# Optimization experiments

Measured on AMD Instinct MI355X. Metric: run time of the kernel, lower is better.

Reference implementation:

```python
import jax, jax.numpy as jnp
import numpy as np

B, D, RES, NSLOTS, NITERS = 32, 256, 64, 8, 3
NTOK = RES * RES
SCALE = D ** -0.5
EPS = 1e-8
LN_EPS = 1e-5


def _ln(x, g, b, axes=(-1,)):
    m = x.mean(axes, keepdims=True)
    v = x.var(axes, keepdims=True)
    return (x - m) / jnp.sqrt(v + LN_EPS) * g + b


def _build_grid(res):
    xy = jnp.linspace(0.0, 1.0, res)
    xx, yy = jnp.meshgrid(xy, xy, indexing='ij')
    g = jnp.stack([xx, yy], axis=-1)[None]  # [1,res,res,2]
    return jnp.concatenate([g, 1.0 - g], axis=-1)  # [1,res,res,4]


GRID = _build_grid(RES)


def setup_inputs() -> dict:
    key = jax.random.key(0)
    ks = iter(jax.random.split(key, 48))
    w = lambda shp: 0.02 * jax.random.normal(next(ks), shp, jnp.float32)
    z = lambda shp: jnp.zeros(shp, jnp.float32)
    o = lambda shp: jnp.ones(shp, jnp.float32)
    return dict(
        x=jax.random.normal(next(ks), (B, D, RES, RES), jnp.float32),
        eps_noise=jax.random.normal(next(ks), (B, NSLOTS, D), jnp.float32),
        pos_w=w((4, D)), pos_b=z((D,)),
        enc_g=o((NTOK, D)), enc_b=z((NTOK, D)),
        fm_w1=w((D, D)), fm_b1=z((D,)), fm_w2=w((D, D)), fm_b2=z((D,)),
        in_g=o((D,)), in_b=z((D,)),
        q_w=w((D, D)), q_b=z((D,)),
        k_w=w((D, D)), k_b=z((D,)),
        v_w=w((D, D)), v_b=z((D,)),
        gru_wih=w((D, 3 * D)), gru_whh=w((D, 3 * D)), gru_bih=z((3 * D,)), gru_bhh=z((3 * D,)),
        pre_g=o((D,)), pre_b=z((D,)),
        st_w1=w((D, D)), st_b1=z((D,)), st_w2=w((D, D)), st_b2=z((D,)),
        slot_g=o((D,)), slot_b=z((D,)),
        slots_loc=w((1, D)),
        slots_logscale=jax.random.uniform(next(ks), (1, D), jnp.float32),
    )


def reference(x, eps_noise, pos_w, pos_b, enc_g, enc_b, fm_w1, fm_b1, fm_w2, fm_b2,
              in_g, in_b, q_w, q_b, k_w, k_b, v_w, v_b,
              gru_wih, gru_whh, gru_bih, gru_bhh, pre_g, pre_b,
              st_w1, st_b1, st_w2, st_b2, slot_g, slot_b, slots_loc, slots_logscale):
    # SoftPositionEmbed: x + Linear(grid) permuted to NCHW
    pos = GRID @ pos_w + pos_b                       # [1,res,res,D]
    h = x + jnp.transpose(pos, (0, 3, 1, 2))         # [B,D,res,res]
    tokens = h.reshape(B, D, NTOK).transpose(0, 2, 1)  # [B,NTOK,D]
    # encoder_norm: LayerNorm over [NTOK, D] jointly
    tokens = _ln(tokens, enc_g, enc_b, axes=(-2, -1))
    tokens = jax.nn.relu(tokens @ fm_w1 + fm_b1)
    tokens = jax.nn.relu(tokens @ fm_w2 + fm_b2)
    tokens = _ln(tokens, in_g, in_b)                 # norm_input
    k = tokens @ k_w + k_b                           # [B,NTOK,D]
    v = tokens @ v_w + v_b
    # stochastic initial slots (non-variational branch)
    slots = slots_loc[None] + jnp.exp(slots_logscale)[None] * eps_noise  # [B,S,D]
    for _ in range(NITERS):
        prev = slots
        s = _ln(slots, slot_g, slot_b)               # norm_slots
        q = s @ q_w + q_b
        dots = jnp.einsum('bid,bjd->bij', q, k) * SCALE  # [B,S,NTOK]
        attn = jax.nn.softmax(dots, axis=1) + EPS    # softmax over SLOT axis
        attn = attn / attn.sum(-1, keepdims=True)    # renormalize over tokens
        upd = jnp.einsum('bij,bjd->bid', attn, v)    # [B,S,D]
        # GRUCell(update, prev) — torch gate order r,z,n
        gi = upd @ gru_wih + gru_bih
        gh = prev @ gru_whh + gru_bhh
        ir, iz, inn = jnp.split(gi, 3, axis=-1)
        hr, hz, hn = jnp.split(gh, 3, axis=-1)
        r = jax.nn.sigmoid(ir + hr)
        zt = jax.nn.sigmoid(iz + hz)
        n = jnp.tanh(inn + r * hn)
        slots = (1.0 - zt) * n + zt * prev
        # residual MLP: slots += slot_transformation(norm_pre_ff(slots))
        ff = _ln(slots, pre_g, pre_b)
        ff = jax.nn.relu(ff @ st_w1 + st_b1)
        ff = jax.nn.relu(ff @ st_w2 + st_b2)
        slots = slots + ff
    return slots
```

## Files before the change

### kernel.cpp

```cpp
#include <hip/hip_runtime.h>
#include <hip/hip_bf16.h>

typedef __attribute__((ext_vector_type(8))) short short8;
typedef __attribute__((ext_vector_type(4))) float f32x4;

#define DEVI static __device__ __forceinline__

DEVI ushort f2bf(float f) {
  union { __hip_bfloat16 h; ushort u; } c; c.h = __float2bfloat16(f); return c.u;
}
DEVI float bf2f(ushort u) {
  union { __hip_bfloat16 h; ushort u; } c; c.u = u; return __bfloat162float(c.h);
}

DEVI void blk_reduce2(float& a, float& b) {
  #pragma unroll
  for (int m = 1; m < 64; m <<= 1) {
    a += __shfl_xor(a, m);
    b += __shfl_xor(b, m);
  }
  __shared__ float sc[8];
  int tid = threadIdx.x, w = tid >> 6;
  if ((tid & 63) == 0) { sc[w * 2] = a; sc[w * 2 + 1] = b; }
  __syncthreads();
  if (tid == 0) {
    sc[0] = sc[0] + sc[2] + sc[4] + sc[6];
    sc[1] = sc[1] + sc[3] + sc[5] + sc[7];
  }
  __syncthreads();
  a = sc[0]; b = sc[1];
  __syncthreads();
}

__global__ void kw_kernel(const float* w0, const float* w1, const float* w2, const float* w3,
                          ushort* wT, float* bstats) {
  int widx = blockIdx.y;
  const float* src = (widx == 0) ? w0 : (widx == 1) ? w1 : (widx == 2) ? w2 : w3;
  ushort* dst = wT + (size_t)widx * 65536;
  int tile = blockIdx.x;
  int k0 = (tile >> 2) * 64, n0 = (tile & 3) * 64;
  __shared__ float t[64][65];
  int tid = threadIdx.x;
  int r = tid >> 2, c0 = (tid & 3) * 16;
  #pragma unroll
  for (int j = 0; j < 16; j += 4) {
    float4 v = *reinterpret_cast<const float4*>(src + (size_t)(k0 + r) * 256 + n0 + c0 + j);
    t[r][c0 + j + 0] = v.x; t[r][c0 + j + 1] = v.y;
    t[r][c0 + j + 2] = v.z; t[r][c0 + j + 3] = v.w;
  }
  __syncthreads();
  ushort buf[16];
  #pragma unroll
  for (int j = 0; j < 16; j++) buf[j] = f2bf(t[c0 + j][r]);
  size_t o = (size_t)(n0 + r) * 256 + k0 + c0;
  *reinterpret_cast<uint4*>(dst + o) = *reinterpret_cast<uint4*>(&buf[0]);
  *reinterpret_cast<uint4*>(dst + o + 8) = *reinterpret_cast<uint4*>(&buf[8]);
  if (blockIdx.x == 0 && blockIdx.y == 0 && tid < 64) bstats[tid] = 0.f;
}

__global__ void k1_stats(const float* x, const float* pos_w, const float* pos_b, float* bstats) {
  int b = blockIdx.y, blk = blockIdx.x, tid = threadIdx.x;
  const float* xb = x + (size_t)b * 1048576;
  float s = 0.f, sq = 0.f;
  for (int i = 0; i < 16; i++) {
    int e4 = blk * 4096 + i * 256 + tid;
    int e = e4 * 4;
    int d = e >> 12, t = e & 4095;
    int ii = t >> 6, j0 = t & 63;
    float xx = ii * (1.f / 63.f);
    float c0 = pos_w[512 + d] + pos_w[768 + d] + pos_b[d];
    float cx = pos_w[d] - pos_w[512 + d];
    float cy = pos_w[256 + d] - pos_w[768 + d];
    float4 v = reinterpret_cast<const float4*>(xb)[e4];
    float base = c0 + xx * cx;
    #pragma unroll
    for (int j = 0; j < 4; j++) {
      float yy = (j0 + j) * (1.f / 63.f);
      float h = (&v.x)[j] + base + yy * cy;
      s += h; sq += h * h;
    }
  }
  blk_reduce2(s, sq);
  if (tid == 0) {
    atomicAdd(&bstats[b * 2], s);
    atomicAdd(&bstats[b * 2 + 1], sq);
  }
}

__global__ void k2_tokens(const float* x, const float* pos_w, const float* pos_b,
                          const float* enc_g, const float* enc_b, const float* bstats,
                          ushort* t0) {
  int tcx = blockIdx.x;
  int dcx = blockIdx.y;
  int b = blockIdx.z;
  int tid = threadIdx.x;
  float mean = bstats[b * 2] * (1.f / 1048576.f);
  float var = bstats[b * 2 + 1] * (1.f / 1048576.f) - mean * mean;
  float rstd = rsqrtf(var + 1e-5f);
  __shared__ float tt[64][65];
  const float* xb = x + (size_t)b * 1048576;
  float xx = tcx * (1.f / 63.f);
  #pragma unroll
  for (int it = 0; it < 4; it++) {
    int idx = tid + it * 256;
    int dl = idx >> 4, f4 = idx & 15;
    int d = dcx * 64 + dl;
    float c0 = pos_w[512 + d] + pos_w[768 + d] + pos_b[d];
    float cx = pos_w[d] - pos_w[512 + d];
    float cy = pos_w[256 + d] - pos_w[768 + d];
    float4 v = *reinterpret_cast<const float4*>(xb + (size_t)d * 4096 + tcx * 64 + f4 * 4);
    float base = c0 + xx * cx;
    #pragma unroll
    for (int j = 0; j < 4; j++) {
      float yy = (f4 * 4 + j) * (1.f / 63.f);
      tt[f4 * 4 + j][dl] = (&v.x)[j] + base + yy * cy;
    }
  }
  __syncthreads();
  int t_l = tid >> 2, dc = (tid & 3) * 16;
  int t = tcx * 64 + t_l;
  ushort ob[16];
  #pragma unroll
  for (int j = 0; j < 16; j++) {
    int d = dcx * 64 + dc + j;
    float h = (tt[t_l][dc + j] - mean) * rstd;
    h = h * enc_g[(size_t)t * 256 + d] + enc_b[(size_t)t * 256 + d];
    ob[j] = f2bf(h);
  }
  size_t o = (size_t)(b * 4096 + t) * 256 + dcx * 64 + dc;
  *reinterpret_cast<uint4*>(t0 + o) = *reinterpret_cast<uint4*>(&ob[0]);
  *reinterpret_cast<uint4*>(t0 + o + 8) = *reinterpret_cast<uint4*>(&ob[8]);
}

template <bool RELU>
__global__ __launch_bounds__(512) void gemm_kernel(const ushort* __restrict__ A,
                                                   const ushort* __restrict__ WT,
                                                   const float* __restrict__ bias,
                                                   ushort* __restrict__ C) {
  __shared__ ushort As[128 * 72];
  __shared__ ushort Bs[256 * 72];
  int tid = threadIdx.x;
  int r0 = blockIdx.x * 128;
  int w = tid >> 6, lane = tid & 63;
  int wr = w >> 2, wc = w & 3;
  f32x4 acc[4][4];
  #pragma unroll
  for (int m = 0; m < 4; m++)
    #pragma unroll
    for (int n = 0; n < 4; n++) acc[m][n] = (f32x4)(0.f);

  for (int ks = 0; ks < 4; ks++) {
    int k0 = ks * 64;
    __syncthreads();
    #pragma unroll
    for (int i = 0; i < 2; i++) {
      int idx = tid + i * 512;
      int r = idx >> 3, cc = idx & 7;
      uint4 v = *reinterpret_cast<const uint4*>(A + (size_t)(r0 + r) * 256 + k0 + cc * 8);
      *reinterpret_cast<uint4*>(&As[r * 72 + cc * 8]) = v;
    }
    #pragma unroll
    for (int i = 0; i < 4; i++) {
      int idx = tid + i * 512;
      int r = idx >> 3, cc = idx & 7;
      uint4 v = *reinterpret_cast<const uint4*>(WT + (size_t)r * 256 + k0 + cc * 8);
      *reinterpret_cast<uint4*>(&Bs[r * 72 + cc * 8]) = v;
    }
    __syncthreads();
    #pragma unroll
    for (int ksub = 0; ksub < 2; ksub++) {
      int kk = ksub * 32 + (lane >> 4) * 8;
      short8 af[4], bf[4];
      #pragma unroll
      for (int m = 0; m < 4; m++)
        af[m] = *reinterpret_cast<const short8*>(&As[(wr * 64 + m * 16 + (lane & 15)) * 72 + kk]);
      #pragma unroll
      for (int n = 0; n < 4; n++)
        bf[n] = *reinterpret_cast<const short8*>(&Bs[(wc * 64 + n * 16 + (lane & 15)) * 72 + kk]);
      #pragma unroll
      for (int m = 0; m < 4; m++)
        #pragma unroll
        for (int n = 0; n < 4; n++)
          acc[m][n] = __builtin_amdgcn_mfma_f32_16x16x32_bf16(af[m], bf[n], acc[m][n], 0, 0, 0);
    }
  }
  #pragma unroll
  for (int m = 0; m < 4; m++) {
    int row = r0 + wr * 64 + m * 16 + ((lane >> 4) << 2);
    #pragma unroll
    for (int n = 0; n < 4; n++) {
      int col = wc * 64 + n * 16 + (lane & 15);
      float bv = bias[col];
      #pragma unroll
      for (int q = 0; q < 4; q++) {
        float v = acc[m][n][q] + bv;
        if (RELU) v = fmaxf(v, 0.f);
        C[(size_t)(row + q) * 256 + col] = f2bf(v);
      }
    }
  }
}

__global__ void lnrow_kernel(ushort* t, const float* g, const float* bta) {
  int row = blockIdx.x * 4 + (threadIdx.x >> 6);
  int lane = threadIdx.x & 63;
  ushort* p = t + (size_t)row * 256 + lane * 4;
  uint2 v = *reinterpret_cast<const uint2*>(p);
  ushort us[4]; *reinterpret_cast<uint2*>(us) = v;
  float f[4];
  float s = 0.f, sq = 0.f;
  #pragma unroll
  for (int j = 0; j < 4; j++) { f[j] = bf2f(us[j]); s += f[j]; sq += f[j] * f[j]; }
  #pragma unroll
  for (int m = 1; m < 64; m <<= 1) { s += __shfl_xor(s, m); sq += __shfl_xor(sq, m); }
  float mean = s * (1.f / 256.f);
  float var = sq * (1.f / 256.f) - mean * mean;
  float rstd = rsqrtf(var + 1e-5f);
  float4 gv = *reinterpret_cast<const float4*>(g + lane * 4);
  float4 bv = *reinterpret_cast<const float4*>(bta + lane * 4);
  #pragma unroll
  for (int j = 0; j < 4; j++) us[j] = f2bf((f[j] - mean) * rstd * (&gv.x)[j] + (&bv.x)[j]);
  *reinterpret_cast<uint2*>(p) = *reinterpret_cast<uint2*>(us);
}

__global__ void kslots_kernel(const float* eps, const float* loc, const float* lsc, float* slots) {
  int i = blockIdx.x * 256 + threadIdx.x;
  int d = i & 255;
  slots[i] = loc[d] + expf(lsc[d]) * eps[i];
}

__global__ void ka_kernel(const float* slots, const float* sg, const float* sb,
                          const float* qw, const float* qb, ushort* qT, float* attn_sum) {
  int s = blockIdx.x;
  int b = blockIdx.y;
  int tid = threadIdx.x;
  ushort* qrow = qT + ((size_t)b * 16 + s) * 256;
  if (s >= 8) { qrow[tid] = 0; return; }
  __shared__ float sn[256];
  float xv = slots[((size_t)b * 8 + s) * 256 + tid];
  float a = xv, sq = xv * xv;
  blk_reduce2(a, sq);
  float mean = a * (1.f / 256.f);
  float var = sq * (1.f / 256.f) - mean * mean;
  float rstd = rsqrtf(var + 1e-5f);
  sn[tid] = (xv - mean) * rstd * sg[tid] + sb[tid];
  __syncthreads();
  float acc = qb[tid];
  for (int d = 0; d < 256; d++) acc = fmaf(sn[d], qw[(size_t)d * 256 + tid], acc);
  qrow[tid] = f2bf(acc * 0.0625f);
  if (tid == 0) attn_sum[b * 8 + s] = 0.f;
}

__global__ __launch_bounds__(256) void kb_kernel(const ushort* __restrict__ kmat,
                                                 const ushort* __restrict__ qT,
                                                 float* __restrict__ attn,
                                                 float* __restrict__ attn_sum,
                                                 float* __restrict__ upd) {
  int tcx = blockIdx.x;
  int b = blockIdx.y;
  int tid = threadIdx.x, w = tid >> 6, lane = tid & 63;
  if (tid < 128) upd[(size_t)b * 2048 + tcx * 128 + tid] = 0.f;
  __shared__ ushort Ks[256 * 72];
  const ushort* kbase = kmat + ((size_t)b * 4096 + tcx * 256) * 256;
  const ushort* qbase = qT + (size_t)b * 16 * 256;
  f32x4 acc[4];
  #pragma unroll
  for (int m = 0; m < 4; m++) acc[m] = (f32x4)(0.f);
  for (int ks = 0; ks < 4; ks++) {
    int k0 = ks * 64;
    __syncthreads();
    #pragma unroll
    for (int i = 0; i < 8; i++) {
      int idx = tid + i * 256;
      int r = idx >> 3, cc = idx & 7;
      *reinterpret_cast<uint4*>(&Ks[r * 72 + cc * 8]) =
          *reinterpret_cast<const uint4*>(kbase + (size_t)r * 256 + k0 + cc * 8);
    }
    __syncthreads();
    #pragma unroll
    for (int ksub = 0; ksub < 2; ksub++) {
      int kk = ksub * 32 + (lane >> 4) * 8;
      short8 bq = *reinterpret_cast<const short8*>(qbase + (lane & 15) * 256 + k0 + kk);
      #pragma unroll
      for (int m = 0; m < 4; m++) {
        short8 af = *reinterpret_cast<const short8*>(&Ks[(w * 64 + m * 16 + (lane & 15)) * 72 + kk]);
        acc[m] = __builtin_amdgcn_mfma_f32_16x16x32_bf16(af, bq, acc[m], 0, 0, 0);
      }
    }
  }
  bool valid = (lane & 15) < 8;
  float lsum = 0.f;
  int srow = (lane >> 4) * 4;
  #pragma unroll
  for (int m = 0; m < 4; m++) {
    #pragma unroll
    for (int q = 0; q < 4; q++) {
      float d = acc[m][q];
      float mv = valid ? d : -1e30f;
      #pragma unroll
      for (int msk = 1; msk < 16; msk <<= 1) mv = fmaxf(mv, __shfl_xor(mv, msk));
      float e = valid ? expf(d - mv) : 0.f;
      float ssum = e;
      #pragma unroll
      for (int msk = 1; msk < 16; msk <<= 1) ssum += __shfl_xor(ssum, msk);
      if (valid) {
        float av = e / ssum + 1e-8f;
        int t = tcx * 256 + w * 64 + m * 16 + srow + q;
        attn[((size_t)b * 4096 + t) * 8 + (lane & 15)] = av;
        lsum += av;
      }
    }
  }
  lsum += __shfl_xor(lsum, 16);
  lsum += __shfl_xor(lsum, 32);
  __shared__ float wsum[4][16];
  if (lane < 16) wsum[w][lane] = lsum;
  __syncthreads();
  if (tid < 8) {
    float tot = wsum[0][tid] + wsum[1][tid] + wsum[2][tid] + wsum[3][tid];
    atomicAdd(&attn_sum[b * 8 + tid], tot);
  }
}

__global__ __launch_bounds__(256) void kc_kernel(const ushort* __restrict__ vmat,
                                                 const float* __restrict__ attn,
                                                 float* __restrict__ upd) {
  int tcx = blockIdx.x;
  int b = blockIdx.y;
  int tid = threadIdx.x, g = tid >> 6, lane = tid & 63;
  __shared__ float at[64][8];
  __shared__ float red[4][8][256];
  float acc[8][4];
  #pragma unroll
  for (int s = 0; s < 8; s++)
    #pragma unroll
    for (int j = 0; j < 4; j++) acc[s][j] = 0.f;
  const ushort* vb = vmat + ((size_t)b * 4096 + tcx * 512) * 256;
  const float* ab = attn + ((size_t)b * 4096 + tcx * 512) * 8;
  for (int tile = 0; tile < 8; tile++) {
    __syncthreads();
    if (tid < 128)
      *reinterpret_cast<float4*>(&at[0][0] + tid * 4) =
          *reinterpret_cast<const float4*>(ab + tile * 512 + tid * 4);
    __syncthreads();
    for (int ti = 0; ti < 16; ti++) {
      int tl = g * 16 + ti;
      uint2 vv = *reinterpret_cast<const uint2*>(vb + (size_t)(tile * 64 + tl) * 256 + lane * 4);
      ushort us[4]; *reinterpret_cast<uint2*>(us) = vv;
      float vf[4];
      #pragma unroll
      for (int j = 0; j < 4; j++) vf[j] = bf2f(us[j]);
      #pragma unroll
      for (int s = 0; s < 8; s++) {
        float a = at[tl][s];
        #pragma unroll
        for (int j = 0; j < 4; j++) acc[s][j] = fmaf(a, vf[j], acc[s][j]);
      }
    }
  }
  #pragma unroll
  for (int s = 0; s < 8; s++) {
    float4 v4; v4.x = acc[s][0]; v4.y = acc[s][1]; v4.z = acc[s][2]; v4.w = acc[s][3];
    *reinterpret_cast<float4*>(&red[g][s][lane * 4]) = v4;
  }
  __syncthreads();
  #pragma unroll
  for (int i = 0; i < 8; i++) {
    int idx = tid + i * 256;
    int s = idx >> 8, d = idx & 255;
    float sum = red[0][s][d] + red[1][s][d] + red[2][s][d] + red[3][s][d];
    atomicAdd(&upd[((size_t)b * 8 + s) * 256 + d], sum);
  }
}

__global__ void kd_kernel(const float* __restrict__ upd, const float* __restrict__ attn_sum,
                          float* __restrict__ slots,
                          const float* __restrict__ wih, const float* __restrict__ whh,
                          const float* __restrict__ bih, const float* __restrict__ bhh,
                          const float* __restrict__ pre_g, const float* __restrict__ pre_b,
                          const float* __restrict__ w1, const float* __restrict__ b1,
                          const float* __restrict__ w2, const float* __restrict__ b2,
                          float* __restrict__ out_extra) {
  int s = blockIdx.x, b = blockIdx.y;
  int tid = threadIdx.x;
  size_t base = ((size_t)b * 8 + s) * 256;
  __shared__ float u[256], p[256], f1[256], f2[256];
  float inv = 1.f / attn_sum[b * 8 + s];
  u[tid] = upd[base + tid] * inv;
  p[tid] = slots[base + tid];
  __syncthreads();
  float gi0 = bih[tid], gi1 = bih[256 + tid], gi2 = bih[512 + tid];
  float gh0 = bhh[tid], gh1 = bhh[256 + tid], gh2 = bhh[512 + tid];
  for (int d = 0; d < 256; d++) {
    float ud = u[d], pd = p[d];
    const float* wi = wih + (size_t)d * 768 + tid;
    const float* wh = whh + (size_t)d * 768 + tid;
    gi0 = fmaf(ud, wi[0], gi0); gi1 = fmaf(ud, wi[256], gi1); gi2 = fmaf(ud, wi[512], gi2);
    gh0 = fmaf(pd, wh[0], gh0); gh1 = fmaf(pd, wh[256], gh1); gh2 = fmaf(pd, wh[512], gh2);
  }
  float r = 1.f / (1.f + expf(-(gi0 + gh0)));
  float z = 1.f / (1.f + expf(-(gi1 + gh1)));
  float n = tanhf(gi2 + r * gh2);
  float hv = (1.f - z) * n + z * p[tid];
  float a = hv, sq = hv * hv;
  blk_reduce2(a, sq);
  float mean = a * (1.f / 256.f);
  float var = sq * (1.f / 256.f) - mean * mean;
  float rstd = rsqrtf(var + 1e-5f);
  f1[tid] = (hv - mean) * rstd * pre_g[tid] + pre_b[tid];
  __syncthreads();
  float acc1 = b1[tid];
  for (int d = 0; d < 256; d++) acc1 = fmaf(f1[d], w1[(size_t)d * 256 + tid], acc1);
  acc1 = fmaxf(acc1, 0.f);
  f2[tid] = acc1;
  __syncthreads();
  float acc2 = b2[tid];
  for (int d = 0; d < 256; d++) acc2 = fmaf(f2[d], w2[(size_t)d * 256 + tid], acc2);
  acc2 = fmaxf(acc2, 0.f);
  float res = hv + acc2;
  slots[base + tid] = res;
  if (out_extra) out_extra[base + tid] = res;
}

extern "C" void kernel_launch(void* const* d_in, const int* in_sizes, int n_in,
                              void* d_out, int out_size, void* d_ws, size_t ws_size,
                              hipStream_t stream) {
  const float* x         = (const float*)d_in[0];
  const float* eps_noise = (const float*)d_in[1];
  const float* pos_w     = (const float*)d_in[2];
  const float* pos_b     = (const float*)d_in[3];
  const float* enc_g     = (const float*)d_in[4];
  const float* enc_b     = (const float*)d_in[5];
  const float* fm_w1     = (const float*)d_in[6];
  const float* fm_b1     = (const float*)d_in[7];
  const float* fm_w2     = (const float*)d_in[8];
  const float* fm_b2     = (const float*)d_in[9];
  const float* in_g      = (const float*)d_in[10];
  const float* in_b      = (const float*)d_in[11];
  const float* q_w       = (const float*)d_in[12];
  const float* q_b       = (const float*)d_in[13];
  const float* k_w       = (const float*)d_in[14];
  const float* k_b       = (const float*)d_in[15];
  const float* v_w       = (const float*)d_in[16];
  const float* v_b       = (const float*)d_in[17];
  const float* gru_wih   = (const float*)d_in[18];
  const float* gru_whh   = (const float*)d_in[19];
  const float* gru_bih   = (const float*)d_in[20];
  const float* gru_bhh   = (const float*)d_in[21];
  const float* pre_g     = (const float*)d_in[22];
  const float* pre_b     = (const float*)d_in[23];
  const float* st_w1     = (const float*)d_in[24];
  const float* st_b1     = (const float*)d_in[25];
  const float* st_w2     = (const float*)d_in[26];
  const float* st_b2     = (const float*)d_in[27];
  const float* slot_g    = (const float*)d_in[28];
  const float* slot_b    = (const float*)d_in[29];
  const float* slots_loc = (const float*)d_in[30];
  const float* slots_lsc = (const float*)d_in[31];
  (void)in_sizes; (void)n_in; (void)out_size;

  char* ws = (char*)d_ws;
  const size_t OFF_BUFB   = 67108864;
  const size_t OFF_WT     = 134217728;
  const size_t OFF_QT     = OFF_WT + 524288;
  const size_t OFF_ATTN   = OFF_QT + 262144;
  const size_t OFF_SLOTS  = OFF_ATTN + 4194304;
  const size_t OFF_UPD    = OFF_SLOTS + 262144;
  const size_t OFF_BSTATS = OFF_UPD + 262144;
  const size_t OFF_ASUM   = OFF_BSTATS + 256;
  const size_t NEED       = OFF_ASUM + 1024;
  if (ws_size < NEED) return;

  ushort* bufA   = (ushort*)ws;
  ushort* bufB   = (ushort*)(ws + OFF_BUFB);
  ushort* wT     = (ushort*)(ws + OFF_WT);
  ushort* qT     = (ushort*)(ws + OFF_QT);
  float* attn    = (float*)(ws + OFF_ATTN);
  float* slots   = (float*)(ws + OFF_SLOTS);
  float* upd     = (float*)(ws + OFF_UPD);
  float* bstats  = (float*)(ws + OFF_BSTATS);
  float* asum    = (float*)(ws + OFF_ASUM);

  kw_kernel<<<dim3(16, 4), 256, 0, stream>>>(fm_w1, fm_w2, k_w, v_w, wT, bstats);
  k1_stats<<<dim3(64, 32), 256, 0, stream>>>(x, pos_w, pos_b, bstats);
  k2_tokens<<<dim3(64, 4, 32), 256, 0, stream>>>(x, pos_w, pos_b, enc_g, enc_b, bstats, bufA);
  gemm_kernel<true><<<1024, 512, 0, stream>>>(bufA, wT, fm_b1, bufA);
  gemm_kernel<true><<<1024, 512, 0, stream>>>(bufA, wT + 65536, fm_b2, bufA);
  lnrow_kernel<<<32768, 256, 0, stream>>>(bufA, in_g, in_b);
  gemm_kernel<false><<<1024, 512, 0, stream>>>(bufA, wT + 131072, k_b, bufB);
  gemm_kernel<false><<<1024, 512, 0, stream>>>(bufA, wT + 196608, v_b, bufA);
  kslots_kernel<<<256, 256, 0, stream>>>(eps_noise, slots_loc, slots_lsc, slots);
  for (int it = 0; it < 3; it++) {
    ka_kernel<<<dim3(16, 32), 256, 0, stream>>>(slots, slot_g, slot_b, q_w, q_b, qT, asum);
    kb_kernel<<<dim3(16, 32), 256, 0, stream>>>(bufB, qT, attn, asum, upd);
    kc_kernel<<<dim3(8, 32), 256, 0, stream>>>(bufA, attn, upd);
    kd_kernel<<<dim3(8, 32), 256, 0, stream>>>(upd, asum, slots,
        gru_wih, gru_whh, gru_bih, gru_bhh, pre_g, pre_b,
        st_w1, st_b1, st_w2, st_b2, (it == 2) ? (float*)d_out : nullptr);
  }
}
```

Before: 743.1 us.

## Fuse LayerNorm into GEMM, merge K/V GEMMs, fuse attention stages, async LDS loads

Folds the row LayerNorm into the second feature-MLP GEMM epilogue and computes the K and V projections in one kernel that shares the A tile. The attention-weight and weighted-sum kernels are merged so the attention matrix stays in shared memory. The next iteration's query projection moves into the GRU/MLP kernel, and the slot-init and first-query kernels are combined. Tile loads switch to direct global-to-LDS loads with unpadded rows, which removes the register staging but may introduce LDS bank conflicts. Together these cut kernel launches and global round trips.

```diff
diff --git a/kernel.cpp b/kernel.cpp
--- a/kernel.cpp
+++ b/kernel.cpp
@@ -11,6 +11,12 @@
 }
 DEVI float bf2f(ushort u) {
   union { __hip_bfloat16 h; ushort u; } c; c.u = u; return __bfloat162float(c.h);
+}
+
+DEVI void gload16(const ushort* g, ushort* l) {
+  __builtin_amdgcn_global_load_lds(
+      (const __attribute__((address_space(1))) void*)g,
+      (__attribute__((address_space(3))) void*)l, 16, 0, 0);
 }
 
 DEVI void blk_reduce2(float& a, float& b) {
@@ -132,13 +138,16 @@
   *reinterpret_cast<uint4*>(t0 + o + 8) = *reinterpret_cast<uint4*>(&ob[8]);
 }
 
-template <bool RELU>
-__global__ __launch_bounds__(512) void gemm_kernel(const ushort* __restrict__ A,
-                                                   const ushort* __restrict__ WT,
-                                                   const float* __restrict__ bias,
-                                                   ushort* __restrict__ C) {
-  __shared__ ushort As[128 * 72];
-  __shared__ ushort Bs[256 * 72];
+template <bool RELU, bool LN>
+__global__ __launch_bounds__(512) void gemm_one(const ushort* __restrict__ A,
+                                                const ushort* __restrict__ WT,
+                                                const float* __restrict__ bias,
+                                                const float* __restrict__ lng,
+                                                const float* __restrict__ lnb,
+                                                ushort* __restrict__ C) {
+  __shared__ __align__(16) ushort As[128 * 64];
+  __shared__ __align__(16) ushort Bs[256 * 64];
+  __shared__ float rstats[128][4][2];
   int tid = threadIdx.x;
   int r0 = blockIdx.x * 128;
   int w = tid >> 6, lane = tid & 63;
@@ -155,16 +164,12 @@
     #pragma unroll
     for (int i = 0; i < 2; i++) {
       int idx = tid + i * 512;
-      int r = idx >> 3, cc = idx & 7;
-      uint4 v = *reinterpret_cast<const uint4*>(A + (size_t)(r0 + r) * 256 + k0 + cc * 8);
-      *reinterpret_cast<uint4*>(&As[r * 72 + cc * 8]) = v;
+      gload16(A + (size_t)(r0 + (idx >> 3)) * 256 + k0 + (idx & 7) * 8, &As[idx * 8]);
     }
     #pragma unroll
     for (int i = 0; i < 4; i++) {
       int idx = tid + i * 512;
-      int r = idx >> 3, cc = idx & 7;
-      uint4 v = *reinterpret_cast<const uint4*>(WT + (size_t)r * 256 + k0 + cc * 8);
-      *reinterpret_cast<uint4*>(&Bs[r * 72 + cc * 8]) = v;
+      gload16(WT + (size_t)(idx >> 3) * 256 + k0 + (idx & 7) * 8, &Bs[idx * 8]);
     }
     __syncthreads();
     #pragma unroll
@@ -173,10 +178,10 @@
       short8 af[4], bf[4];
       #pragma unroll
       for (int m = 0; m < 4; m++)
-        af[m] = *reinterpret_cast<const short8*>(&As[(wr * 64 + m * 16 + (lane & 15)) * 72 + kk]);
+        af[m] = *reinterpret_cast<const short8*>(&As[(wr * 64 + m * 16 + (lane & 15)) * 64 + kk]);
       #pragma unroll
       for (int n = 0; n < 4; n++)
-        bf[n] = *reinterpret_cast<const short8*>(&Bs[(wc * 64 + n * 16 + (lane & 15)) * 72 + kk]);
+        bf[n] = *reinterpret_cast<const short8*>(&Bs[(wc * 64 + n * 16 + (lane & 15)) * 64 + kk]);
       #pragma unroll
       for (int m = 0; m < 4; m++)
         #pragma unroll
@@ -184,83 +189,176 @@
           acc[m][n] = __builtin_amdgcn_mfma_f32_16x16x32_bf16(af[m], bf[n], acc[m][n], 0, 0, 0);
     }
   }
+  float bcol[4], gcol[4], ocol[4];
+  #pragma unroll
+  for (int n = 0; n < 4; n++) {
+    int col = wc * 64 + n * 16 + (lane & 15);
+    bcol[n] = bias[col];
+    if (LN) { gcol[n] = lng[col]; ocol[n] = lnb[col]; }
+  }
+  #pragma unroll
+  for (int m = 0; m < 4; m++)
+    #pragma unroll
+    for (int n = 0; n < 4; n++)
+      #pragma unroll
+      for (int q = 0; q < 4; q++) {
+        float v = acc[m][n][q] + bcol[n];
+        if (RELU) v = fmaxf(v, 0.f);
+        acc[m][n][q] = v;
+      }
+  if (LN) {
+    #pragma unroll
+    for (int m = 0; m < 4; m++)
+      #pragma unroll
+      for (int q = 0; q < 4; q++) {
+        float rs = 0.f, rq = 0.f;
+        #pragma unroll
+        for (int n = 0; n < 4; n++) { float v = acc[m][n][q]; rs += v; rq += v * v; }
+        #pragma unroll
+        for (int msk = 1; msk < 16; msk <<= 1) { rs += __shfl_xor(rs, msk); rq += __shfl_xor(rq, msk); }
+        if ((lane & 15) == 0) {
+          int lr = wr * 64 + m * 16 + (lane >> 4) * 4 + q;
+          rstats[lr][wc][0] = rs; rstats[lr][wc][1] = rq;
+        }
+      }
+    __syncthreads();
+    #pragma unroll
+    for (int m = 0; m < 4; m++)
+      #pragma unroll
+      for (int q = 0; q < 4; q++) {
+        int lr = wr * 64 + m * 16 + (lane >> 4) * 4 + q;
+        float s = rstats[lr][0][0] + rstats[lr][1][0] + rstats[lr][2][0] + rstats[lr][3][0];
+        float ssq = rstats[lr][0][1] + rstats[lr][1][1] + rstats[lr][2][1] + rstats[lr][3][1];
+        float mean = s * (1.f / 256.f);
+        float rstd = rsqrtf(ssq * (1.f / 256.f) - mean * mean + 1e-5f);
+        #pragma unroll
+        for (int n = 0; n < 4; n++)
+          acc[m][n][q] = (acc[m][n][q] - mean) * rstd * gcol[n] + ocol[n];
+      }
+  }
   #pragma unroll
   for (int m = 0; m < 4; m++) {
     int row = r0 + wr * 64 + m * 16 + ((lane >> 4) << 2);
     #pragma unroll
     for (int n = 0; n < 4; n++) {
       int col = wc * 64 + n * 16 + (lane & 15);
-      float bv = bias[col];
+      #pragma unroll
+      for (int q = 0; q < 4; q++)
+        C[(size_t)(row + q) * 256 + col] = f2bf(acc[m][n][q]);
+    }
+  }
+}
+
+__global__ __launch_bounds__(512) void gemm_kv(const ushort* __restrict__ A,
+                                               const ushort* __restrict__ WTk,
+                                               const ushort* __restrict__ WTv,
+                                               const float* __restrict__ bk,
+                                               const float* __restrict__ bv,
+                                               ushort* __restrict__ Ck,
+                                               ushort* __restrict__ Cv) {
+  __shared__ __align__(16) ushort As[128 * 64];
+  __shared__ __align__(16) ushort Bs1[256 * 64];
+  __shared__ __align__(16) ushort Bs2[256 * 64];
+  int tid = threadIdx.x;
+  int r0 = blockIdx.x * 128;
+  int w = tid >> 6, lane = tid & 63;
+  int wr = w >> 2, wc = w & 3;
+  f32x4 acc1[4][4], acc2[4][4];
+  #pragma unroll
+  for (int m = 0; m < 4; m++)
+    #pragma unroll
+    for (int n = 0; n < 4; n++) { acc1[m][n] = (f32x4)(0.f); acc2[m][n] = (f32x4)(0.f); }
+
+  for (int ks = 0; ks < 4; ks++) {
+    int k0 = ks * 64;
+    __syncthreads();
+    #pragma unroll
+    for (int i = 0; i < 2; i++) {
+      int idx = tid + i * 512;
+      gload16(A + (size_t)(r0 + (idx >> 3)) * 256 + k0 + (idx & 7) * 8, &As[idx * 8]);
+    }
+    #pragma unroll
+    for (int i = 0; i < 4; i++) {
+      int idx = tid + i * 512;
+      gload16(WTk + (size_t)(idx >> 3) * 256 + k0 + (idx & 7) * 8, &Bs1[idx * 8]);
+    }
+    #pragma unroll
+    for (int i = 0; i < 4; i++) {
+      int idx = tid + i * 512;
+      gload16(WTv + (size_t)(idx >> 3) * 256 + k0 + (idx & 7) * 8, &Bs2[idx * 8]);
+    }
+    __syncthreads();
+    #pragma unroll
+    for (int ksub = 0; ksub < 2; ksub++) {
+      int kk = ksub * 32 + (lane >> 4) * 8;
+      short8 af[4], bf1[4], bf2[4];
+      #pragma unroll
+      for (int m = 0; m < 4; m++)
+        af[m] = *reinterpret_cast<const short8*>(&As[(wr * 64 + m * 16 + (lane & 15)) * 64 + kk]);
+      #pragma unroll
+      for (int n = 0; n < 4; n++) {
+        bf1[n] = *reinterpret_cast<const short8*>(&Bs1[(wc * 64 + n * 16 + (lane & 15)) * 64 + kk]);
+        bf2[n] = *reinterpret_cast<const short8*>(&Bs2[(wc * 64 + n * 16 + (lane & 15)) * 64 + kk]);
+      }
+      #pragma unroll
+      for (int m = 0; m < 4; m++)
+        #pragma unroll
+        for (int n = 0; n < 4; n++) {
+          acc1[m][n] = __builtin_amdgcn_mfma_f32_16x16x32_bf16(af[m], bf1[n], acc1[m][n], 0, 0, 0);
+          acc2[m][n] = __builtin_amdgcn_mfma_f32_16x16x32_bf16(af[m], bf2[n], acc2[m][n], 0, 0, 0);
+        }
+    }
+  }
+  #pragma unroll
+  for (int m = 0; m < 4; m++) {
+    int row = r0 + wr * 64 + m * 16 + ((lane >> 4) << 2);
+    #pragma unroll
+    for (int n = 0; n < 4; n++) {
+      int col = wc * 64 + n * 16 + (lane & 15);
+      float b1 = bk[col], b2 = bv[col];
       #pragma unroll
       for (int q = 0; q < 4; q++) {
-        float v = acc[m][n][q] + bv;
-        if (RELU) v = fmaxf(v, 0.f);
-        C[(size_t)(row + q) * 256 + col] = f2bf(v);
-      }
-    }
-  }
-}
-
-__global__ void lnrow_kernel(ushort* t, const float* g, const float* bta) {
-  int row = blockIdx.x * 4 + (threadIdx.x >> 6);
-  int lane = threadIdx.x & 63;
-  ushort* p = t + (size_t)row * 256 + lane * 4;
-  uint2 v = *reinterpret_cast<const uint2*>(p);
-  ushort us[4]; *reinterpret_cast<uint2*>(us) = v;
-  float f[4];
-  float s = 0.f, sq = 0.f;
-  #pragma unroll
-  for (int j = 0; j < 4; j++) { f[j] = bf2f(us[j]); s += f[j]; sq += f[j] * f[j]; }
-  #pragma unroll
-  for (int m = 1; m < 64; m <<= 1) { s += __shfl_xor(s, m); sq += __shfl_xor(sq, m); }
-  float mean = s * (1.f / 256.f);
-  float var = sq * (1.f / 256.f) - mean * mean;
-  float rstd = rsqrtf(var + 1e-5f);
-  float4 gv = *reinterpret_cast<const float4*>(g + lane * 4);
-  float4 bv = *reinterpret_cast<const float4*>(bta + lane * 4);
-  #pragma unroll
-  for (int j = 0; j < 4; j++) us[j] = f2bf((f[j] - mean) * rstd * (&gv.x)[j] + (&bv.x)[j]);
-  *reinterpret_cast<uint2*>(p) = *reinterpret_cast<uint2*>(us);
-}
-
-__global__ void kslots_kernel(const float* eps, const float* loc, const float* lsc, float* slots) {
-  int i = blockIdx.x * 256 + threadIdx.x;
-  int d = i & 255;
-  slots[i] = loc[d] + expf(lsc[d]) * eps[i];
-}
-
-__global__ void ka_kernel(const float* slots, const float* sg, const float* sb,
-                          const float* qw, const float* qb, ushort* qT, float* attn_sum) {
-  int s = blockIdx.x;
-  int b = blockIdx.y;
-  int tid = threadIdx.x;
-  ushort* qrow = qT + ((size_t)b * 16 + s) * 256;
-  if (s >= 8) { qrow[tid] = 0; return; }
+        Ck[(size_t)(row + q) * 256 + col] = f2bf(acc1[m][n][q] + b1);
+        Cv[(size_t)(row + q) * 256 + col] = f2bf(acc2[m][n][q] + b2);
+      }
+    }
+  }
+}
+
+__global__ void kslots_q(const float* eps, const float* loc, const float* lsc,
+                         const float* sg, const float* sb,
+                         const float* qw, const float* qb,
+                         float* slots, ushort* qT, float* upd, float* asum) {
+  int s = blockIdx.x, b = blockIdx.y, tid = threadIdx.x;
+  size_t base = ((size_t)b * 8 + s) * 256;
+  float val = loc[tid] + expf(lsc[tid]) * eps[base + tid];
+  slots[base + tid] = val;
+  upd[base + tid] = 0.f;
+  qT[((size_t)b * 16 + 8 + s) * 256 + tid] = 0;
+  if (tid == 0) asum[b * 8 + s] = 0.f;
   __shared__ float sn[256];
-  float xv = slots[((size_t)b * 8 + s) * 256 + tid];
-  float a = xv, sq = xv * xv;
+  float a = val, sq = val * val;
   blk_reduce2(a, sq);
   float mean = a * (1.f / 256.f);
-  float var = sq * (1.f / 256.f) - mean * mean;
-  float rstd = rsqrtf(var + 1e-5f);
-  sn[tid] = (xv - mean) * rstd * sg[tid] + sb[tid];
-  __syncthreads();
-  float acc = qb[tid];
-  for (int d = 0; d < 256; d++) acc = fmaf(sn[d], qw[(size_t)d * 256 + tid], acc);
-  qrow[tid] = f2bf(acc * 0.0625f);
-  if (tid == 0) attn_sum[b * 8 + s] = 0.f;
-}
-
-__global__ __launch_bounds__(256) void kb_kernel(const ushort* __restrict__ kmat,
-                                                 const ushort* __restrict__ qT,
-                                                 float* __restrict__ attn,
-                                                 float* __restrict__ attn_sum,
-                                                 float* __restrict__ upd) {
+  float rstd = rsqrtf(sq * (1.f / 256.f) - mean * mean + 1e-5f);
+  sn[tid] = (val - mean) * rstd * sg[tid] + sb[tid];
+  __syncthreads();
+  float qacc = qb[tid];
+  for (int d = 0; d < 256; d++) qacc = fmaf(sn[d], qw[(size_t)d * 256 + tid], qacc);
+  qT[((size_t)b * 16 + s) * 256 + tid] = f2bf(qacc * 0.0625f);
+}
+
+__global__ __launch_bounds__(256) void kbc_kernel(const ushort* __restrict__ kmat,
+                                                  const ushort* __restrict__ vmat,
+                                                  const ushort* __restrict__ qT,
+                                                  float* __restrict__ attn_sum,
+                                                  float* __restrict__ upd) {
   int tcx = blockIdx.x;
   int b = blockIdx.y;
   int tid = threadIdx.x, w = tid >> 6, lane = tid & 63;
-  if (tid < 128) upd[(size_t)b * 2048 + tcx * 128 + tid] = 0.f;
-  __shared__ ushort Ks[256 * 72];
+  __shared__ __align__(16) ushort Ks[256 * 64];
+  __shared__ float at[256][9];
+  __shared__ float wsum[4][16];
   const ushort* kbase = kmat + ((size_t)b * 4096 + tcx * 256) * 256;
   const ushort* qbase = qT + (size_t)b * 16 * 256;
   f32x4 acc[4];
@@ -272,9 +370,7 @@
     #pragma unroll
     for (int i = 0; i < 8; i++) {
       int idx = tid + i * 256;
-      int r = idx >> 3, cc = idx & 7;
-      *reinterpret_cast<uint4*>(&Ks[r * 72 + cc * 8]) =
-          *reinterpret_cast<const uint4*>(kbase + (size_t)r * 256 + k0 + cc * 8);
+      gload16(kbase + (size_t)(idx >> 3) * 256 + k0 + (idx & 7) * 8, &Ks[idx * 8]);
     }
     __syncthreads();
     #pragma unroll
@@ -283,7 +379,7 @@
       short8 bq = *reinterpret_cast<const short8*>(qbase + (lane & 15) * 256 + k0 + kk);
       #pragma unroll
       for (int m = 0; m < 4; m++) {
-        short8 af = *reinterpret_cast<const short8*>(&Ks[(w * 64 + m * 16 + (lane & 15)) * 72 + kk]);
+        short8 af = *reinterpret_cast<const short8*>(&Ks[(w * 64 + m * 16 + (lane & 15)) * 64 + kk]);
         acc[m] = __builtin_amdgcn_mfma_f32_16x16x32_bf16(af, bq, acc[m], 0, 0, 0);
       }
     }
@@ -305,63 +401,45 @@
       for (int msk = 1; msk < 16; msk <<= 1) ssum += __shfl_xor(ssum, msk);
       if (valid) {
         float av = e / ssum + 1e-8f;
-        int t = tcx * 256 + w * 64 + m * 16 + srow + q;
-        attn[((size_t)b * 4096 + t) * 8 + (lane & 15)] = av;
+        int t = w * 64 + m * 16 + srow + q;
+        at[t][lane & 15] = av;
         lsum += av;
       }
     }
   }
   lsum += __shfl_xor(lsum, 16);
   lsum += __shfl_xor(lsum, 32);
-  __shared__ float wsum[4][16];
   if (lane < 16) wsum[w][lane] = lsum;
   __syncthreads();
   if (tid < 8) {
     float tot = wsum[0][tid] + wsum[1][tid] + wsum[2][tid] + wsum[3][tid];
     atomicAdd(&attn_sum[b * 8 + tid], tot);
   }
-}
-
-__global__ __launch_bounds__(256) void kc_kernel(const ushort* __restrict__ vmat,
-                                                 const float* __restrict__ attn,
-                                                 float* __restrict__ upd) {
-  int tcx = blockIdx.x;
-  int b = blockIdx.y;
-  int tid = threadIdx.x, g = tid >> 6, lane = tid & 63;
-  __shared__ float at[64][8];
-  __shared__ float red[4][8][256];
-  float acc[8][4];
+  float pacc[8][4];
   #pragma unroll
   for (int s = 0; s < 8; s++)
     #pragma unroll
-    for (int j = 0; j < 4; j++) acc[s][j] = 0.f;
-  const ushort* vb = vmat + ((size_t)b * 4096 + tcx * 512) * 256;
-  const float* ab = attn + ((size_t)b * 4096 + tcx * 512) * 8;
-  for (int tile = 0; tile < 8; tile++) {
-    __syncthreads();
-    if (tid < 128)
-      *reinterpret_cast<float4*>(&at[0][0] + tid * 4) =
-          *reinterpret_cast<const float4*>(ab + tile * 512 + tid * 4);
-    __syncthreads();
-    for (int ti = 0; ti < 16; ti++) {
-      int tl = g * 16 + ti;
-      uint2 vv = *reinterpret_cast<const uint2*>(vb + (size_t)(tile * 64 + tl) * 256 + lane * 4);
-      ushort us[4]; *reinterpret_cast<uint2*>(us) = vv;
-      float vf[4];
-      #pragma unroll
-      for (int j = 0; j < 4; j++) vf[j] = bf2f(us[j]);
-      #pragma unroll
-      for (int s = 0; s < 8; s++) {
-        float a = at[tl][s];
-        #pragma unroll
-        for (int j = 0; j < 4; j++) acc[s][j] = fmaf(a, vf[j], acc[s][j]);
-      }
-    }
-  }
+    for (int j = 0; j < 4; j++) pacc[s][j] = 0.f;
+  const ushort* vb = vmat + ((size_t)b * 4096 + tcx * 256) * 256;
+  for (int ti = 0; ti < 64; ti++) {
+    int t = w * 64 + ti;
+    uint2 vv = *reinterpret_cast<const uint2*>(vb + (size_t)t * 256 + lane * 4);
+    ushort us[4]; *reinterpret_cast<uint2*>(us) = vv;
+    float vf[4];
+    #pragma unroll
+    for (int j = 0; j < 4; j++) vf[j] = bf2f(us[j]);
+    #pragma unroll
+    for (int s = 0; s < 8; s++) {
+      float a = at[t][s];
+      #pragma unroll
+      for (int j = 0; j < 4; j++) pacc[s][j] = fmaf(a, vf[j], pacc[s][j]);
+    }
+  }
+  float (*red)[8][256] = reinterpret_cast<float (*)[8][256]>(Ks);
   #pragma unroll
   for (int s = 0; s < 8; s++) {
-    float4 v4; v4.x = acc[s][0]; v4.y = acc[s][1]; v4.z = acc[s][2]; v4.w = acc[s][3];
-    *reinterpret_cast<float4*>(&red[g][s][lane * 4]) = v4;
+    float4 v4; v4.x = pacc[s][0]; v4.y = pacc[s][1]; v4.z = pacc[s][2]; v4.w = pacc[s][3];
+    *reinterpret_cast<float4*>(&red[w][s][lane * 4]) = v4;
   }
   __syncthreads();
   #pragma unroll
@@ -373,24 +451,28 @@
   }
 }
 
-__global__ void kd_kernel(const float* __restrict__ upd, const float* __restrict__ attn_sum,
+__global__ void kd_kernel(const float* __restrict__ upd_in, const float* __restrict__ attn_sum,
                           float* __restrict__ slots,
                           const float* __restrict__ wih, const float* __restrict__ whh,
                           const float* __restrict__ bih, const float* __restrict__ bhh,
                           const float* __restrict__ pre_g, const float* __restrict__ pre_b,
                           const float* __restrict__ w1, const float* __restrict__ b1,
                           const float* __restrict__ w2, const float* __restrict__ b2,
-                          float* __restrict__ out_extra) {
+                          const float* __restrict__ sg, const float* __restrict__ sb,
+                          const float* __restrict__ qw, const float* __restrict__ qb,
+                          ushort* __restrict__ qT_next, float* __restrict__ upd_clear,
+                          float* __restrict__ asum_clear, float* __restrict__ out_final) {
   int s = blockIdx.x, b = blockIdx.y;
   int tid = threadIdx.x;
   size_t base = ((size_t)b * 8 + s) * 256;
   __shared__ float u[256], p[256], f1[256], f2[256];
   float inv = 1.f / attn_sum[b * 8 + s];
-  u[tid] = upd[base + tid] * inv;
+  u[tid] = upd_in[base + tid] * inv;
   p[tid] = slots[base + tid];
   __syncthreads();
   float gi0 = bih[tid], gi1 = bih[256 + tid], gi2 = bih[512 + tid];
   float gh0 = bhh[tid], gh1 = bhh[256 + tid], gh2 = bhh[512 + tid];
+  #pragma unroll 4
   for (int d = 0; d < 256; d++) {
     float ud = u[d], pd = p[d];
     const float* wi = wih + (size_t)d * 768 + tid;
@@ -405,21 +487,37 @@
   float a = hv, sq = hv * hv;
   blk_reduce2(a, sq);
   float mean = a * (1.f / 256.f);
-  float var = sq * (1.f / 256.f) - mean * mean;
-  float rstd = rsqrtf(var + 1e-5f);
+  float rstd = rsqrtf(sq * (1.f / 256.f) - mean * mean + 1e-5f);
   f1[tid] = (hv - mean) * rstd * pre_g[tid] + pre_b[tid];
   __syncthreads();
   float acc1 = b1[tid];
+  #pragma unroll 4
   for (int d = 0; d < 256; d++) acc1 = fmaf(f1[d], w1[(size_t)d * 256 + tid], acc1);
   acc1 = fmaxf(acc1, 0.f);
   f2[tid] = acc1;
   __syncthreads();
   float acc2 = b2[tid];
+  #pragma unroll 4
   for (int d = 0; d < 256; d++) acc2 = fmaf(f2[d], w2[(size_t)d * 256 + tid], acc2);
   acc2 = fmaxf(acc2, 0.f);
   float res = hv + acc2;
   slots[base + tid] = res;
-  if (out_extra) out_extra[base + tid] = res;
+  if (qT_next == nullptr) {
+    out_final[base + tid] = res;
+    return;
+  }
+  float a2 = res, sq2 = res * res;
+  blk_reduce2(a2, sq2);
+  float mean2 = a2 * (1.f / 256.f);
+  float rstd2 = rsqrtf(sq2 * (1.f / 256.f) - mean2 * mean2 + 1e-5f);
+  f1[tid] = (res - mean2) * rstd2 * sg[tid] + sb[tid];
+  __syncthreads();
+  float qacc = qb[tid];
+  #pragma unroll 4
+  for (int d = 0; d < 256; d++) qacc = fmaf(f1[d], qw[(size_t)d * 256 + tid], qacc);
+  qT_next[((size_t)b * 16 + s) * 256 + tid] = f2bf(qacc * 0.0625f);
+  upd_clear[base + tid] = 0.f;
+  if (tid == 0) asum_clear[b * 8 + s] = 0.f;
 }
 
 extern "C" void kernel_launch(void* const* d_in, const int* in_sizes, int n_in,
@@ -463,8 +561,7 @@
   const size_t OFF_BUFB   = 67108864;
   const size_t OFF_WT     = 134217728;
   const size_t OFF_QT     = OFF_WT + 524288;
-  const size_t OFF_ATTN   = OFF_QT + 262144;
-  const size_t OFF_SLOTS  = OFF_ATTN + 4194304;
+  const size_t OFF_SLOTS  = OFF_QT + 262144;
   const size_t OFF_UPD    = OFF_SLOTS + 262144;
   const size_t OFF_BSTATS = OFF_UPD + 262144;
   const size_t OFF_ASUM   = OFF_BSTATS + 256;
@@ -475,7 +572,6 @@
   ushort* bufB   = (ushort*)(ws + OFF_BUFB);
   ushort* wT     = (ushort*)(ws + OFF_WT);
   ushort* qT     = (ushort*)(ws + OFF_QT);
-  float* attn    = (float*)(ws + OFF_ATTN);
   float* slots   = (float*)(ws + OFF_SLOTS);
   float* upd     = (float*)(ws + OFF_UPD);
   float* bstats  = (float*)(ws + OFF_BSTATS);
@@ -484,18 +580,17 @@
   kw_kernel<<<dim3(16, 4), 256, 0, stream>>>(fm_w1, fm_w2, k_w, v_w, wT, bstats);
   k1_stats<<<dim3(64, 32), 256, 0, stream>>>(x, pos_w, pos_b, bstats);
   k2_tokens<<<dim3(64, 4, 32), 256, 0, stream>>>(x, pos_w, pos_b, enc_g, enc_b, bstats, bufA);
-  gemm_kernel<true><<<1024, 512, 0, stream>>>(bufA, wT, fm_b1, bufA);
-  gemm_kernel<true><<<1024, 512, 0, stream>>>(bufA, wT + 65536, fm_b2, bufA);
-  lnrow_kernel<<<32768, 256, 0, stream>>>(bufA, in_g, in_b);
-  gemm_kernel<false><<<1024, 512, 0, stream>>>(bufA, wT + 131072, k_b, bufB);
-  gemm_kernel<false><<<1024, 512, 0, stream>>>(bufA, wT + 196608, v_b, bufA);
-  kslots_kernel<<<256, 256, 0, stream>>>(eps_noise, slots_loc, slots_lsc, slots);
+  gemm_one<true, false><<<1024, 512, 0, stream>>>(bufA, wT, fm_b1, nullptr, nullptr, bufA);
+  gemm_one<true, true><<<1024, 512, 0, stream>>>(bufA, wT + 65536, fm_b2, in_g, in_b, bufA);
+  gemm_kv<<<1024, 512, 0, stream>>>(bufA, wT + 131072, wT + 196608, k_b, v_b, bufB, bufA);
+  kslots_q<<<dim3(8, 32), 256, 0, stream>>>(eps_noise, slots_loc, slots_lsc, slot_g, slot_b,
+                                            q_w, q_b, slots, qT, upd, asum);
   for (int it = 0; it < 3; it++) {
-    ka_kernel<<<dim3(16, 32), 256, 0, stream>>>(slots, slot_g, slot_b, q_w, q_b, qT, asum);
-    kb_kernel<<<dim3(16, 32), 256, 0, stream>>>(bufB, qT, attn, asum, upd);
-    kc_kernel<<<dim3(8, 32), 256, 0, stream>>>(bufA, attn, upd);
+    kbc_kernel<<<dim3(16, 32), 256, 0, stream>>>(bufB, bufA, qT, asum, upd);
+    bool last = (it == 2);
     kd_kernel<<<dim3(8, 32), 256, 0, stream>>>(upd, asum, slots,
         gru_wih, gru_whh, gru_bih, gru_bhh, pre_g, pre_b,
-        st_w1, st_b1, st_w2, st_b2, (it == 2) ? (float*)d_out : nullptr);
-  }
-}
+        st_w1, st_b1, st_w2, st_b2, slot_g, slot_b, q_w, q_b,
+        last ? nullptr : qT, upd, asum, last ? (float*)d_out : nullptr);
+  }
+}
```

Measured after the change: 805.2 us. 8.4% more time.
